# Optimization experiments

Hardware: AMD Instinct MI355X
Metric: run time of the kernel (lower is better)

Reference implementation:

```python
import jax, jax.numpy as jnp
import numpy as np

GROUP_SIZE = 128
# AWQ nibble unpack order: reverse_awq_order = [0,4,1,5,2,6,3,7]; shifts = order*4
AWQ_SHIFTS = jnp.array([0, 16, 4, 20, 8, 24, 12, 28], dtype=jnp.int32)


def awq_dequantize(qweight, scales, qzeros, group_size=GROUP_SIZE):
    # qweight: [K, N//8] int32, scales: [K//g, N] f32, qzeros: [K//g, N//8] int32
    K = qweight.shape[0]
    N = scales.shape[1]
    # unpack 8 4-bit values per int32 in AWQ order -> [K, N]
    w = ((qweight[:, :, None] >> AWQ_SHIFTS) & 15).reshape(K, N).astype(scales.dtype)
    z = ((qzeros[:, :, None] >> AWQ_SHIFTS) & 15).reshape(-1, N).astype(scales.dtype)
    # broadcast per-group scales/zeros along the K (row) axis
    z_full = jnp.repeat(z, group_size, axis=0)       # [K, N]
    s_full = jnp.repeat(scales, group_size, axis=0)  # [K, N]
    return (w - z_full) * s_full                      # [K, N]


def setup_inputs() -> dict:
    key = jax.random.key(0)
    k1, k2, k3, k4 = jax.random.split(key, 4)
    K, N, g = 4096, 11008, GROUP_SIZE
    x = jax.random.normal(k1, (4096, K), dtype=jnp.float32)
    qweight = jax.random.randint(k2, (K, N // 8), 0, 2147483647, dtype=jnp.int32)
    scales = jax.random.uniform(k3, (K // g, N), dtype=jnp.float32) * 0.01
    qzeros = jax.random.randint(k4, (K // g, N // 8), 0, 2147483647, dtype=jnp.int32)
    return {"x": x, "qweight": qweight, "scales": scales, "qzeros": qzeros}


def reference(x, qweight, scales, qzeros):
    # F.linear(x, W_deq.T) == x @ W_deq, W_deq: [K, N]
    w_deq = awq_dequantize(qweight, scales, qzeros)
    return x @ w_deq  # [tokens, N]
```

## Files before the change

kernel.cpp:

```cpp
#include <hip/hip_runtime.h>
#include <hip/hip_fp16.h>
#include <stdint.h>
#include <stddef.h>

#define MM 4096
#define NN 11008
#define KK 4096
#define NQ (NN / 8)

#define BM 256
#define BN 256
#define BK 32
#define NKT (KK / BK)
#define GRID_N (NN / BN)
#define GRID_M (MM / BM)
#define NWG (GRID_N * GRID_M)

typedef _Float16 half8 __attribute__((ext_vector_type(8)));
typedef _Float16 half2v __attribute__((ext_vector_type(2)));
typedef float f32x4 __attribute__((ext_vector_type(4)));
typedef uint32_t uint4v __attribute__((ext_vector_type(4)));

union U1H2 { uint32_t u; half2v h; };
union U4H8 { uint4v u; half8 h; };

__device__ __forceinline__ void gload_lds16(const void* g, void* l) {
  __builtin_amdgcn_global_load_lds(
      (const __attribute__((address_space(1))) uint32_t*)g,
      (__attribute__((address_space(3))) uint32_t*)l, 16, 0, 0);
}

__global__ __launch_bounds__(256) void convert_x_kernel(const float* __restrict__ x,
                                                        _Float16* __restrict__ xh) {
  const int idx = (blockIdx.x * 256 + threadIdx.x) * 8;
  const float4* p = reinterpret_cast<const float4*>(x + idx);
  float4 a = p[0], b = p[1];
  U4H8 r;
  r.h[0] = (_Float16)a.x; r.h[1] = (_Float16)a.y;
  r.h[2] = (_Float16)a.z; r.h[3] = (_Float16)a.w;
  r.h[4] = (_Float16)b.x; r.h[5] = (_Float16)b.y;
  r.h[6] = (_Float16)b.z; r.h[7] = (_Float16)b.w;
  *reinterpret_cast<uint4v*>(xh + idx) = r.u;
}

__global__ __launch_bounds__(256) void dequant_w_kernel(const uint32_t* __restrict__ qw,
                                                        const float* __restrict__ sc,
                                                        const uint32_t* __restrict__ qz,
                                                        _Float16* __restrict__ w1) {
  const int T = blockIdx.x * 256 + threadIdx.x;
  const int qc = T % NQ;
  const int kb8 = T / NQ;
  const int g = kb8 >> 4;

  const uint32_t* qp = qw + (size_t)(kb8 * 8) * NQ + qc;
  uint32_t q[8];
#pragma unroll
  for (int j = 0; j < 8; ++j) q[j] = qp[(size_t)j * NQ];

  const uint32_t zq = qz[(size_t)g * NQ + qc];
  const float* sp = sc + (size_t)g * NN + qc * 8;
  float4 s0 = *reinterpret_cast<const float4*>(sp);
  float4 s1 = *reinterpret_cast<const float4*>(sp + 4);
  const float sv[8] = {s0.x, s0.y, s0.z, s0.w, s1.x, s1.y, s1.z, s1.w};

  _Float16* op = w1 + ((size_t)kb8 * NN + (size_t)qc * 8) * 8;
#pragma unroll
  for (int c = 0; c < 8; ++c) {
    const int sh = ((c >> 1) << 2) + ((c & 1) << 4);
    uint32_t zc = ((zq >> sh) & 15u) | 0x6400u;
    zc |= zc << 16;
    U1H2 uz; uz.u = zc;
    const _Float16 hs = (_Float16)sv[c];
    half2v s2 = {hs, hs};
    uint4v outp;
#pragma unroll
    for (int i = 0; i < 4; ++i) {
      const uint32_t lo = (q[2 * i] >> sh) & 15u;
      const uint32_t hi = (q[2 * i + 1] >> sh) & 15u;
      U1H2 uw; uw.u = lo | (hi << 16) | 0x64006400u;
      U1H2 ur; ur.h = (uw.h - uz.h) * s2;
      outp[i] = ur.u;
    }
    *reinterpret_cast<uint4v*>(op + c * 8) = outp;
  }
}

__global__ __launch_bounds__(512, 2)
void gemm_pipe(const _Float16* __restrict__ xh, const _Float16* __restrict__ w1,
               float* __restrict__ out) {
  __shared__ __align__(16) _Float16 As[4][BM][BK];
  __shared__ __align__(16) _Float16 Bs[4][4][BN][8];

  const int tid = threadIdx.x;
  const int lane = tid & 63;
  const int wid = tid >> 6;
  const int wm = wid >> 2;
  const int wn = wid & 3;
  const int lr = lane & 15;
  const int lq = lane >> 4;

  const int wg = blockIdx.x;
  const int xcd = wg & 7;
  const int j = wg >> 3;
  const int m0 = (xcd * 2 + (j & 1)) * BM;
  const int n0 = (j >> 1) * BN;

  const int ca0 = tid, ca1 = 512 + tid;
  const _Float16* aSrc0 = xh + (size_t)(m0 + (ca0 >> 2)) * KK
                             + ((ca0 & 3) ^ ((ca0 >> 3) & 3)) * 8;
  const _Float16* aSrc1 = xh + (size_t)(m0 + (ca1 >> 2)) * KK
                             + ((ca1 & 3) ^ ((ca1 >> 3) & 3)) * 8;
  const _Float16* bSrc0 = w1 + ((size_t)(ca0 >> 8) * NN + n0 + (ca0 & 255)) * 8;
  const _Float16* bSrc1 = w1 + ((size_t)(ca1 >> 8) * NN + n0 + (ca1 & 255)) * 8;
  const int ldsOffA0 = (wid * 64) * 8;
  const int ldsOffA1 = (512 + wid * 64) * 8;

  const int sa = (lq ^ ((lr >> 1) & 3)) * 8;

  f32x4 acc[8][4];
  const f32x4 fz = {0.f, 0.f, 0.f, 0.f};
#pragma unroll
  for (int i = 0; i < 8; ++i)
#pragma unroll
    for (int jn = 0; jn < 4; ++jn) acc[i][jn] = fz;

#pragma unroll
  for (int t = 0; t < 3; ++t) {
    gload_lds16(aSrc0 + t * BK, (char*)&As[t][0][0] + ldsOffA0 * 2);
    gload_lds16(aSrc1 + t * BK, (char*)&As[t][0][0] + ldsOffA1 * 2);
    gload_lds16(bSrc0 + (size_t)t * NN * 32, (char*)&Bs[t][0][0][0] + ldsOffA0 * 2);
    gload_lds16(bSrc1 + (size_t)t * NN * 32, (char*)&Bs[t][0][0][0] + ldsOffA1 * 2);
  }
  asm volatile("s_waitcnt vmcnt(8)" ::: "memory");
  __builtin_amdgcn_s_barrier();
  __builtin_amdgcn_sched_barrier(0);

  for (int t = 0; t < NKT; ++t) {
    const int b = t & 3;
    const int s = (t + 3) & (NKT - 1);
    const int sb = s & 3;

    half8 af[4], bf[4];
#pragma unroll
    for (int mi = 0; mi < 4; ++mi)
      af[mi] = *reinterpret_cast<const half8*>(&As[b][wm * 128 + mi * 16 + lr][sa]);
#pragma unroll
    for (int ni = 0; ni < 4; ++ni)
      bf[ni] = *reinterpret_cast<const half8*>(&Bs[b][lq][wn * 64 + ni * 16 + lr][0]);
    gload_lds16(aSrc0 + s * BK, (char*)&As[sb][0][0] + ldsOffA0 * 2);
    gload_lds16(aSrc1 + s * BK, (char*)&As[sb][0][0] + ldsOffA1 * 2);
    __builtin_amdgcn_s_barrier();
    asm volatile("s_waitcnt lgkmcnt(0)" ::: "memory");
    __builtin_amdgcn_sched_barrier(0);
    __builtin_amdgcn_s_setprio(1);
#pragma unroll
    for (int mi = 0; mi < 4; ++mi)
#pragma unroll
      for (int ni = 0; ni < 4; ++ni)
        acc[mi][ni] = __builtin_amdgcn_mfma_f32_16x16x32_f16(af[mi], bf[ni], acc[mi][ni], 0, 0, 0);
    __builtin_amdgcn_s_setprio(0);
    __builtin_amdgcn_s_barrier();
    __builtin_amdgcn_sched_barrier(0);

    half8 ag[4];
#pragma unroll
    for (int mi = 0; mi < 4; ++mi)
      ag[mi] = *reinterpret_cast<const half8*>(&As[b][wm * 128 + 64 + mi * 16 + lr][sa]);
    gload_lds16(bSrc0 + (size_t)s * NN * 32, (char*)&Bs[sb][0][0][0] + ldsOffA0 * 2);
    gload_lds16(bSrc1 + (size_t)s * NN * 32, (char*)&Bs[sb][0][0][0] + ldsOffA1 * 2);
    __builtin_amdgcn_s_barrier();
    asm volatile("s_waitcnt lgkmcnt(0)" ::: "memory");
    __builtin_amdgcn_sched_barrier(0);
    __builtin_amdgcn_s_setprio(1);
#pragma unroll
    for (int mi = 0; mi < 4; ++mi)
#pragma unroll
      for (int ni = 0; ni < 4; ++ni)
        acc[4 + mi][ni] = __builtin_amdgcn_mfma_f32_16x16x32_f16(ag[mi], bf[ni], acc[4 + mi][ni], 0, 0, 0);
    __builtin_amdgcn_s_setprio(0);
    asm volatile("s_waitcnt vmcnt(8)" ::: "memory");
    __builtin_amdgcn_s_barrier();
    __builtin_amdgcn_sched_barrier(0);
  }

  float* op = out + (size_t)(m0 + wm * 128) * NN + (n0 + wn * 64);
#pragma unroll
  for (int mi = 0; mi < 8; ++mi)
#pragma unroll
    for (int ni = 0; ni < 4; ++ni)
#pragma unroll
      for (int i = 0; i < 4; ++i) {
        const int row = mi * 16 + lq * 4 + i;
        const int col = ni * 16 + lr;
        op[(size_t)row * NN + col] = acc[mi][ni][i];
      }
}

template <bool APRE>
__global__ __launch_bounds__(256)
void awq_gemm(const float* __restrict__ x, const _Float16* __restrict__ xh,
              const uint32_t* __restrict__ qw, const float* __restrict__ sc,
              const uint32_t* __restrict__ qz, float* __restrict__ out) {
  __shared__ __align__(16) _Float16 Asf[128 * 64];
  __shared__ __align__(16) _Float16 Bsf[128 * 64];

  const int tid = threadIdx.x;
  const int lane = tid & 63;
  const int wid = tid >> 6;
  const int wr = wid >> 1;
  const int wc = wid & 1;
  const int n0 = blockIdx.x * 128;
  const int m0 = blockIdx.y * 128;
  const int lr = lane & 15;
  const int lq = lane >> 4;

  const int bn = tid & 127;
  const int bh = tid >> 7;
  const int gn = n0 + bn;
  const int qc = gn >> 3;
  const int jj = gn & 7;
  const int shift = ((jj >> 1) << 2) + ((jj & 1) << 4);

  const int ar = tid >> 1;
  const int ah = tid & 1;

  f32x4 acc[4][4];
  const f32x4 fz = {0.f, 0.f, 0.f, 0.f};
#pragma unroll
  for (int i = 0; i < 4; ++i)
#pragma unroll
    for (int jn = 0; jn < 4; ++jn) acc[i][jn] = fz;

  half2v zsp = {(_Float16)0.f, (_Float16)0.f};
  half2v ssp = {(_Float16)0.f, (_Float16)0.f};

  for (int kt = 0; kt < KK / 64; ++kt) {
    const int k0 = kt * 64;
    if ((kt & 1) == 0) {
      const int g = k0 >> 7;
      const uint32_t zq = qz[(size_t)g * NQ + qc];
      uint32_t zm = ((zq >> shift) & 15u) | 0x6400u;
      zm |= zm << 16;
      U1H2 uz; uz.u = zm; zsp = uz.h;
      const float s = sc[(size_t)g * NN + gn];
      const _Float16 hs = (_Float16)s;
      ssp[0] = hs; ssp[1] = hs;
    }
    __syncthreads();
    if (APRE) {
#pragma unroll
      for (int i = 0; i < 4; ++i) {
        const int cbase = (i * 4 + wid) * 64;
        const int chunk = cbase + lane;
        const int mrow = chunk >> 3;
        const int slot = (chunk & 7) ^ (mrow & 7);
        const _Float16* gp = xh + (size_t)(m0 + mrow) * KK + k0 + slot * 8;
        gload_lds16(gp, (void*)&Asf[cbase * 8]);
      }
    } else {
      const float* xp = x + (size_t)(m0 + ar) * KK + k0 + ah * 32;
#pragma unroll
      for (int j2 = 0; j2 < 4; ++j2) {
        float4 a4 = *reinterpret_cast<const float4*>(xp + j2 * 8);
        float4 b4 = *reinterpret_cast<const float4*>(xp + j2 * 8 + 4);
        U4H8 r;
        r.h[0] = (_Float16)a4.x; r.h[1] = (_Float16)a4.y;
        r.h[2] = (_Float16)a4.z; r.h[3] = (_Float16)a4.w;
        r.h[4] = (_Float16)b4.x; r.h[5] = (_Float16)b4.y;
        r.h[6] = (_Float16)b4.z; r.h[7] = (_Float16)b4.w;
        const int slot = (ah * 4 + j2) ^ (ar & 7);
        *reinterpret_cast<uint4v*>(&Asf[ar * 64 + slot * 8]) = r.u;
      }
    }
    {
      const uint32_t* qp = qw + (size_t)(k0 + bh * 32) * NQ + qc;
#pragma unroll
      for (int f = 0; f < 4; ++f) {
        uint32_t qv[8];
#pragma unroll
        for (int jv = 0; jv < 8; ++jv) qv[jv] = qp[(size_t)(f * 8 + jv) * NQ];
        uint4v wp;
#pragma unroll
        for (int p = 0; p < 4; ++p) {
          const uint32_t lo = (qv[2 * p] >> shift) & 15u;
          const uint32_t hi = (qv[2 * p + 1] >> shift);
          const uint32_t w01 = (((hi << 16) | lo) & 0x000F000Fu) | 0x64006400u;
          U1H2 uw; uw.u = w01;
          U1H2 ur; ur.h = (uw.h - zsp) * ssp;
          wp[p] = ur.u;
        }
        const int slot = (bh * 4 + f) ^ (bn & 7);
        *reinterpret_cast<uint4v*>(&Bsf[bn * 64 + slot * 8]) = wp;
      }
    }
    __syncthreads();
#pragma unroll
    for (int kq = 0; kq < 2; ++kq) {
      half8 af[4], bf[4];
#pragma unroll
      for (int mi = 0; mi < 4; ++mi) {
        const int am = wr * 64 + mi * 16 + lr;
        const int aslot = (kq * 4 + lq) ^ (am & 7);
        af[mi] = *reinterpret_cast<const half8*>(&Asf[am * 64 + aslot * 8]);
      }
#pragma unroll
      for (int ni = 0; ni < 4; ++ni) {
        const int bn2 = wc * 64 + ni * 16 + lr;
        const int bslot = (kq * 4 + lq) ^ (bn2 & 7);
        bf[ni] = *reinterpret_cast<const half8*>(&Bsf[bn2 * 64 + bslot * 8]);
      }
#pragma unroll
      for (int mi = 0; mi < 4; ++mi)
#pragma unroll
        for (int ni = 0; ni < 4; ++ni)
          acc[mi][ni] = __builtin_amdgcn_mfma_f32_16x16x32_f16(af[mi], bf[ni], acc[mi][ni], 0, 0, 0);
    }
  }

  float* op = out + (size_t)(m0 + wr * 64) * NN + (n0 + wc * 64);
#pragma unroll
  for (int mi = 0; mi < 4; ++mi)
#pragma unroll
    for (int ni = 0; ni < 4; ++ni)
#pragma unroll
      for (int i = 0; i < 4; ++i) {
        const int row = mi * 16 + lq * 4 + i;
        const int col = ni * 16 + lr;
        op[(size_t)row * NN + col] = acc[mi][ni][i];
      }
}

extern "C" void kernel_launch(void* const* d_in, const int* in_sizes, int n_in,
                              void* d_out, int out_size, void* d_ws, size_t ws_size,
                              hipStream_t stream) {
  const float* x = (const float*)d_in[0];
  const uint32_t* qw = (const uint32_t*)d_in[1];
  const float* sc = (const float*)d_in[2];
  const uint32_t* qz = (const uint32_t*)d_in[3];
  float* out = (float*)d_out;

  const size_t xh_bytes = (size_t)MM * KK * sizeof(_Float16);
  const size_t w1_bytes = (size_t)KK * NN * sizeof(_Float16);

  if (ws_size >= xh_bytes + w1_bytes) {
    _Float16* xh = (_Float16*)d_ws;
    _Float16* w1 = (_Float16*)((char*)d_ws + xh_bytes);
    convert_x_kernel<<<(MM * KK) / (256 * 8), 256, 0, stream>>>(x, xh);
    dequant_w_kernel<<<(KK / 8) * NQ / 256, 256, 0, stream>>>(qw, sc, qz, w1);
    gemm_pipe<<<NWG, 512, 0, stream>>>(xh, w1, out);
  } else if (ws_size >= xh_bytes) {
    _Float16* xh = (_Float16*)d_ws;
    convert_x_kernel<<<(MM * KK) / (256 * 8), 256, 0, stream>>>(x, xh);
    awq_gemm<true><<<dim3(NN / 128, MM / 128), 256, 0, stream>>>(x, xh, qw, sc, qz, out);
  } else {
    awq_gemm<false><<<dim3(NN / 128, MM / 128), 256, 0, stream>>>(x, nullptr, qw, sc, qz, out);
  }
}
```

Before: 418.1 us.

## Load B fragments directly from global into registers and double-buffer A fragments

Drops the shared-memory staging buffer for the pre-dequantized B operand. Each wave now reads its B MFMA fragments straight from global memory into registers, one k-tile ahead. The main loop is unrolled by four with ping-pong register sets for the A and B fragments, so the next tile's A reads from shared memory overlap the current MFMAs, and the wait counts are retuned to match. This removes LDS write/read traffic and LDS space for B. In exchange, B global-load latency has only one k-step to hide, waves that share columns load the same B data twice, and register pressure rises.

```diff
diff --git a/kernel.cpp b/kernel.cpp
--- a/kernel.cpp
+++ b/kernel.cpp
@@ -89,7 +89,6 @@
 void gemm_pipe(const _Float16* __restrict__ xh, const _Float16* __restrict__ w1,
                float* __restrict__ out) {
   __shared__ __align__(16) _Float16 As[4][BM][BK];
-  __shared__ __align__(16) _Float16 Bs[4][4][BN][8];
 
   const int tid = threadIdx.x;
   const int lane = tid & 63;
@@ -110,12 +109,12 @@
                              + ((ca0 & 3) ^ ((ca0 >> 3) & 3)) * 8;
   const _Float16* aSrc1 = xh + (size_t)(m0 + (ca1 >> 2)) * KK
                              + ((ca1 & 3) ^ ((ca1 >> 3) & 3)) * 8;
-  const _Float16* bSrc0 = w1 + ((size_t)(ca0 >> 8) * NN + n0 + (ca0 & 255)) * 8;
-  const _Float16* bSrc1 = w1 + ((size_t)(ca1 >> 8) * NN + n0 + (ca1 & 255)) * 8;
-  const int ldsOffA0 = (wid * 64) * 8;
-  const int ldsOffA1 = (512 + wid * 64) * 8;
+  const int dOff0 = wid * 1024;
+  const int dOff1 = 8192 + wid * 1024;
 
   const int sa = (lq ^ ((lr >> 1) & 3)) * 8;
+
+  const _Float16* bFragBase = w1 + ((size_t)lq * NN + n0 + wn * 64 + lr) * 8;
 
   f32x4 acc[8][4];
   const f32x4 fz = {0.f, 0.f, 0.f, 0.f};
@@ -124,64 +123,70 @@
 #pragma unroll
     for (int jn = 0; jn < 4; ++jn) acc[i][jn] = fz;
 
+  half8 af0[4], ag0[4], bf0[4], af1[4], ag1[4], bf1[4];
+
+#pragma unroll
+  for (int ni = 0; ni < 4; ++ni)
+    bf0[ni] = *reinterpret_cast<const half8*>(bFragBase + ni * 128);
 #pragma unroll
   for (int t = 0; t < 3; ++t) {
-    gload_lds16(aSrc0 + t * BK, (char*)&As[t][0][0] + ldsOffA0 * 2);
-    gload_lds16(aSrc1 + t * BK, (char*)&As[t][0][0] + ldsOffA1 * 2);
-    gload_lds16(bSrc0 + (size_t)t * NN * 32, (char*)&Bs[t][0][0][0] + ldsOffA0 * 2);
-    gload_lds16(bSrc1 + (size_t)t * NN * 32, (char*)&Bs[t][0][0][0] + ldsOffA1 * 2);
-  }
-  asm volatile("s_waitcnt vmcnt(8)" ::: "memory");
+    gload_lds16(aSrc0 + t * BK, (char*)&As[t][0][0] + dOff0);
+    gload_lds16(aSrc1 + t * BK, (char*)&As[t][0][0] + dOff1);
+  }
+  asm volatile("s_waitcnt vmcnt(4)" ::: "memory");
   __builtin_amdgcn_s_barrier();
   __builtin_amdgcn_sched_barrier(0);
-
-  for (int t = 0; t < NKT; ++t) {
-    const int b = t & 3;
-    const int s = (t + 3) & (NKT - 1);
-    const int sb = s & 3;
-
-    half8 af[4], bf[4];
-#pragma unroll
-    for (int mi = 0; mi < 4; ++mi)
-      af[mi] = *reinterpret_cast<const half8*>(&As[b][wm * 128 + mi * 16 + lr][sa]);
-#pragma unroll
-    for (int ni = 0; ni < 4; ++ni)
-      bf[ni] = *reinterpret_cast<const half8*>(&Bs[b][lq][wn * 64 + ni * 16 + lr][0]);
-    gload_lds16(aSrc0 + s * BK, (char*)&As[sb][0][0] + ldsOffA0 * 2);
-    gload_lds16(aSrc1 + s * BK, (char*)&As[sb][0][0] + ldsOffA1 * 2);
-    __builtin_amdgcn_s_barrier();
-    asm volatile("s_waitcnt lgkmcnt(0)" ::: "memory");
-    __builtin_amdgcn_sched_barrier(0);
-    __builtin_amdgcn_s_setprio(1);
-#pragma unroll
-    for (int mi = 0; mi < 4; ++mi)
-#pragma unroll
-      for (int ni = 0; ni < 4; ++ni)
-        acc[mi][ni] = __builtin_amdgcn_mfma_f32_16x16x32_f16(af[mi], bf[ni], acc[mi][ni], 0, 0, 0);
-    __builtin_amdgcn_s_setprio(0);
-    __builtin_amdgcn_s_barrier();
-    __builtin_amdgcn_sched_barrier(0);
-
-    half8 ag[4];
-#pragma unroll
-    for (int mi = 0; mi < 4; ++mi)
-      ag[mi] = *reinterpret_cast<const half8*>(&As[b][wm * 128 + 64 + mi * 16 + lr][sa]);
-    gload_lds16(bSrc0 + (size_t)s * NN * 32, (char*)&Bs[sb][0][0][0] + ldsOffA0 * 2);
-    gload_lds16(bSrc1 + (size_t)s * NN * 32, (char*)&Bs[sb][0][0][0] + ldsOffA1 * 2);
-    __builtin_amdgcn_s_barrier();
-    asm volatile("s_waitcnt lgkmcnt(0)" ::: "memory");
-    __builtin_amdgcn_sched_barrier(0);
-    __builtin_amdgcn_s_setprio(1);
-#pragma unroll
-    for (int mi = 0; mi < 4; ++mi)
-#pragma unroll
-      for (int ni = 0; ni < 4; ++ni)
-        acc[4 + mi][ni] = __builtin_amdgcn_mfma_f32_16x16x32_f16(ag[mi], bf[ni], acc[4 + mi][ni], 0, 0, 0);
-    __builtin_amdgcn_s_setprio(0);
-    asm volatile("s_waitcnt vmcnt(8)" ::: "memory");
-    __builtin_amdgcn_s_barrier();
-    __builtin_amdgcn_sched_barrier(0);
-  }
+#pragma unroll
+  for (int mi = 0; mi < 4; ++mi)
+    af0[mi] = *reinterpret_cast<const half8*>(&As[0][wm * 128 + mi * 16 + lr][sa]);
+
+#define TILE_STEP(T0, BUF, SBUF, NBUF, AF, AG, BF, AFN, BFN)                    \
+  {                                                                             \
+    _Pragma("unroll") for (int mi = 0; mi < 4; ++mi)                            \
+      AG[mi] = *reinterpret_cast<const half8*>(                                 \
+          &As[BUF][wm * 128 + 64 + mi * 16 + lr][sa]);                          \
+    gload_lds16(aSrc0 + (size_t)(((T0) + 3) & (NKT - 1)) * BK,                  \
+                (char*)&As[SBUF][0][0] + dOff0);                                \
+    gload_lds16(aSrc1 + (size_t)(((T0) + 3) & (NKT - 1)) * BK,                  \
+                (char*)&As[SBUF][0][0] + dOff1);                                \
+    asm volatile("s_waitcnt vmcnt(2)" ::: "memory");                            \
+    __builtin_amdgcn_s_barrier();                                               \
+    asm volatile("s_waitcnt lgkmcnt(4)" ::: "memory");                          \
+    __builtin_amdgcn_sched_barrier(0);                                          \
+    __builtin_amdgcn_s_setprio(1);                                              \
+    _Pragma("unroll") for (int mi = 0; mi < 4; ++mi)                            \
+      _Pragma("unroll") for (int ni = 0; ni < 4; ++ni)                          \
+        acc[mi][ni] = __builtin_amdgcn_mfma_f32_16x16x32_f16(                   \
+            AF[mi], BF[ni], acc[mi][ni], 0, 0, 0);                              \
+    __builtin_amdgcn_s_setprio(0);                                              \
+    _Pragma("unroll") for (int mi = 0; mi < 4; ++mi)                            \
+      AFN[mi] = *reinterpret_cast<const half8*>(                                \
+          &As[NBUF][wm * 128 + mi * 16 + lr][sa]);                              \
+    {                                                                           \
+      const _Float16* bp =                                                      \
+          bFragBase + (size_t)(((T0) + 1) & (NKT - 1)) * ((size_t)NN * 4 * 8);  \
+      _Pragma("unroll") for (int ni = 0; ni < 4; ++ni)                          \
+        BFN[ni] = *reinterpret_cast<const half8*>(bp + ni * 128);               \
+    }                                                                           \
+    __builtin_amdgcn_s_barrier();                                               \
+    asm volatile("s_waitcnt lgkmcnt(4)" ::: "memory");                          \
+    __builtin_amdgcn_sched_barrier(0);                                          \
+    __builtin_amdgcn_s_setprio(1);                                              \
+    _Pragma("unroll") for (int mi = 0; mi < 4; ++mi)                            \
+      _Pragma("unroll") for (int ni = 0; ni < 4; ++ni)                          \
+        acc[4 + mi][ni] = __builtin_amdgcn_mfma_f32_16x16x32_f16(               \
+            AG[mi], BF[ni], acc[4 + mi][ni], 0, 0, 0);                          \
+    __builtin_amdgcn_s_setprio(0);                                              \
+  }
+
+  for (int v = 0; v < NKT / 4; ++v) {
+    const int t0 = v * 4;
+    TILE_STEP(t0 + 0, 0, 3, 1, af0, ag0, bf0, af1, bf1)
+    TILE_STEP(t0 + 1, 1, 0, 2, af1, ag1, bf1, af0, bf0)
+    TILE_STEP(t0 + 2, 2, 1, 3, af0, ag0, bf0, af1, bf1)
+    TILE_STEP(t0 + 3, 3, 2, 0, af1, ag1, bf1, af0, bf0)
+  }
+#undef TILE_STEP
 
   float* op = out + (size_t)(m0 + wm * 128) * NN + (n0 + wn * 64);
 #pragma unroll
```

Result: faster. 401.0 us (-4.1%).
